# Kernel tuning notes

Hardware: AMD Instinct MI355X
Metric: run time of the kernel (lower is better)

The kernel has to match this reference:

```python
import jax, jax.numpy as jnp
import numpy as np

B, S, H, K, E, C = 4, 1024, 1024, 8, 512, 10000

def setup_inputs() -> dict:
    key = jax.random.key(0)
    ks = jax.random.split(key, 5)
    context = jax.random.normal(ks[0], (B, S, H), dtype=jnp.float32)
    prior_w = jax.random.normal(ks[1], (K, H), dtype=jnp.float32) * 0.02
    prior_b = jnp.zeros((K,), dtype=jnp.float32)
    latent_w = jax.random.normal(ks[2], (K * E, H), dtype=jnp.float32) * 0.02
    latent_b = jnp.zeros((K * E,), dtype=jnp.float32)
    dec_w = jax.random.normal(ks[3], (C, E), dtype=jnp.float32) * 0.02
    dec_b = jnp.zeros((C,), dtype=jnp.float32)
    return {"context": context, "prior_w": prior_w, "prior_b": prior_b,
            "latent_w": latent_w, "latent_b": latent_b,
            "dec_w": dec_w, "dec_b": dec_b}

def reference(context, prior_w, prior_b, latent_w, latent_b, dec_w, dec_b):
    # priors: softmax over components  [B,S,K]
    priors = jax.nn.softmax(jnp.einsum('bsh,kh->bsk', context, prior_w) + prior_b, axis=-1)
    # latent: [B,S,K,E] after tanh (dropout is identity at inference, dropoutl=0)
    latent = jnp.tanh((jnp.einsum('bsh,eh->bse', context, latent_w) + latent_b)
                      .reshape(B, S, K, E))
    # decoder logits + per-component softmax over classes  [B,S,K,C]
    probs = jax.nn.softmax(jnp.einsum('bske,ce->bskc', latent, dec_w) + dec_b, axis=-1)
    # mixture-weighted sum over components  [B,S,C]
    return jnp.einsum('bsk,bskc->bsc', priors, probs)
```

## Files before the change

### kernel.cpp

```cpp
#include <hip/hip_runtime.h>
#include <hip/hip_bf16.h>


#define BM 128
#define BN 128
#define BK 64

typedef __attribute__((ext_vector_type(8))) short bf16x8;
typedef __attribute__((ext_vector_type(4))) float f32x4;

typedef const __attribute__((address_space(1))) unsigned int* gas_u32p;
typedef __attribute__((address_space(3))) unsigned int* las_u32p;

__device__ __forceinline__ unsigned short f2bf(float x) {
  union { float f; unsigned int u; } un; un.f = x;
  unsigned int r = un.u + 0x7FFFu + ((un.u >> 16) & 1u);
  return (unsigned short)(r >> 16);
}

__global__ void k_cvt_bf16(const float4* __restrict__ src, ushort4* __restrict__ dst, int n4) {
  int i = blockIdx.x * blockDim.x + threadIdx.x;
  if (i < n4) {
    float4 v = src[i];
    ushort4 o;
    o.x = f2bf(v.x); o.y = f2bf(v.y); o.z = f2bf(v.z); o.w = f2bf(v.w);
    dst[i] = o;
  }
}

__global__ void k_priors(const float* __restrict__ ctx, const float* __restrict__ pw,
                         const float* __restrict__ pb, float* __restrict__ priors) {
  int t = blockIdx.x;
  int lane = threadIdx.x;
  __shared__ float logit[8];
  const float* c = ctx + (size_t)t * 1024;
  for (int k = 0; k < 8; ++k) {
    const float* w = pw + k * 1024;
    float s = 0.f;
    for (int h = lane; h < 1024; h += 64) s += c[h] * w[h];
    #pragma unroll
    for (int m = 1; m <= 32; m <<= 1) s += __shfl_xor(s, m);
    if (lane == 0) logit[k] = s + pb[k];
  }
  __syncthreads();
  if (lane == 0) {
    float mx = logit[0];
    for (int k = 1; k < 8; ++k) mx = fmaxf(mx, logit[k]);
    float z = 0.f, e[8];
    for (int k = 0; k < 8; ++k) { e[k] = __expf(logit[k] - mx); z += e[k]; }
    float inv = 1.f / z;
    for (int k = 0; k < 8; ++k) priors[(size_t)t * 8 + k] = e[k] * inv;
  }
}

__device__ __forceinline__ void gemm_mainloop(
    const unsigned short* __restrict__ A, const unsigned short* __restrict__ B,
    int lda, int ldb, int m0, int n0, int ktiles,
    unsigned short* ldsA, unsigned short* ldsB, f32x4 acc[4][4]) {
  const int tid = threadIdx.x;
  const int lane = tid & 63;
  const int wave = tid >> 6;
  const int wm = wave & 1, wn = wave >> 1;
  const int lrow = lane & 15, lq = lane >> 4;

  for (int kt = 0; kt < ktiles; ++kt) {
    int k0 = kt * BK;
    __syncthreads();
    #pragma unroll
    for (int p = 0; p < 4; ++p) {
      int chunk = p * 256 + tid;
      int row = chunk >> 3, kc = chunk & 7;
      int kcs = kc ^ (row & 7);
      __builtin_amdgcn_global_load_lds(
          (gas_u32p)(A + (size_t)(m0 + row) * lda + k0 + kcs * 8),
          (las_u32p)(ldsA + chunk * 8), 16, 0, 0);
      __builtin_amdgcn_global_load_lds(
          (gas_u32p)(B + (size_t)(n0 + row) * ldb + k0 + kcs * 8),
          (las_u32p)(ldsB + chunk * 8), 16, 0, 0);
    }
    __syncthreads();
    #pragma unroll
    for (int s = 0; s < 2; ++s) {
      int cbyteoff = (((s * 4 + lq) ^ (lrow & 7)) * 8);
      bf16x8 af[4], bfr[4];
      #pragma unroll
      for (int f = 0; f < 4; ++f)
        af[f] = *(const bf16x8*)(ldsA + (wm * 64 + f * 16 + lrow) * BK + cbyteoff);
      #pragma unroll
      for (int f = 0; f < 4; ++f)
        bfr[f] = *(const bf16x8*)(ldsB + (wn * 64 + f * 16 + lrow) * BK + cbyteoff);
      #pragma unroll
      for (int fi = 0; fi < 4; ++fi)
        #pragma unroll
        for (int fj = 0; fj < 4; ++fj)
          acc[fi][fj] = __builtin_amdgcn_mfma_f32_16x16x32_bf16(af[fi], bfr[fj], acc[fi][fj], 0, 0, 0);
    }
  }
}

__global__ __launch_bounds__(256, 4)
void k_latent(const unsigned short* __restrict__ ctxb, const unsigned short* __restrict__ lwb,
              const float* __restrict__ lb, unsigned short* __restrict__ latent) {
  __shared__ unsigned short lds[(BM + BN) * BK];
  f32x4 zero = {0.f, 0.f, 0.f, 0.f};
  f32x4 acc[4][4];
  #pragma unroll
  for (int i = 0; i < 4; ++i)
    #pragma unroll
    for (int j = 0; j < 4; ++j) acc[i][j] = zero;
  int l = blockIdx.x;
  int xcd = l & 7, idx = l >> 3;
  int ctl = idx & 3, by = idx >> 2;
  int m0 = by * BM, n0 = (xcd * 4 + ctl) * BN;
  gemm_mainloop(ctxb, lwb, 1024, 1024, m0, n0, 1024 / BK, lds, lds + BM * BK, acc);

  const int lane = threadIdx.x & 63, wave = threadIdx.x >> 6;
  const int wm = wave & 1, wn = wave >> 1, lrow = lane & 15, lq = lane >> 4;
  #pragma unroll
  for (int fi = 0; fi < 4; ++fi)
    #pragma unroll
    for (int fj = 0; fj < 4; ++fj) {
      int gcol = n0 + wn * 64 + fj * 16 + lrow;
      float bias = lb[gcol];
      #pragma unroll
      for (int r = 0; r < 4; ++r) {
        int grow = m0 + wm * 64 + fi * 16 + lq * 4 + r;
        float v = tanhf(acc[fi][fj][r] + bias);
        latent[(size_t)grow * 4096 + gcol] = f2bf(v);
      }
    }
}

__global__ __launch_bounds__(256, 4)
void k_dec_pass1(const unsigned short* __restrict__ latb, const unsigned short* __restrict__ dwb,
                 const float* __restrict__ db, float* __restrict__ Z) {
  __shared__ unsigned short lds[(BM + BN) * BK];
  int l = blockIdx.x;
  int xcd = l & 7, idx = l >> 3;
  int ctl = idx % 10, by = idx / 10;
  int n0 = (xcd * 10 + ctl) * BN, m0 = by * BM;
  if (n0 >= 10000) return;

  f32x4 zero = {0.f, 0.f, 0.f, 0.f};
  f32x4 acc[4][4];
  #pragma unroll
  for (int i = 0; i < 4; ++i)
    #pragma unroll
    for (int j = 0; j < 4; ++j) acc[i][j] = zero;
  gemm_mainloop(latb, dwb, 512, 512, m0, n0, 512 / BK, lds, lds + BM * BK, acc);

  const int lane = threadIdx.x & 63, wave = threadIdx.x >> 6;
  const int wm = wave & 1, wn = wave >> 1, lrow = lane & 15, lq = lane >> 4;
  float rowsum[4][4];
  #pragma unroll
  for (int fi = 0; fi < 4; ++fi)
    #pragma unroll
    for (int r = 0; r < 4; ++r) rowsum[fi][r] = 0.f;
  #pragma unroll
  for (int fj = 0; fj < 4; ++fj) {
    int gcol = n0 + wn * 64 + fj * 16 + lrow;
    bool valid = gcol < 10000;
    float bias = valid ? db[gcol] : 0.f;
    #pragma unroll
    for (int fi = 0; fi < 4; ++fi)
      #pragma unroll
      for (int r = 0; r < 4; ++r)
        if (valid) rowsum[fi][r] += __expf(acc[fi][fj][r] + bias);
  }
  #pragma unroll
  for (int fi = 0; fi < 4; ++fi)
    #pragma unroll
    for (int r = 0; r < 4; ++r) {
      float s = rowsum[fi][r];
      s += __shfl_xor(s, 1); s += __shfl_xor(s, 2);
      s += __shfl_xor(s, 4); s += __shfl_xor(s, 8);
      if (lrow == 0) atomicAdd(&Z[m0 + wm * 64 + fi * 16 + lq * 4 + r], s);
    }
}

__global__ __launch_bounds__(256, 4)
void k_dec_pass2(const unsigned short* __restrict__ latb, const unsigned short* __restrict__ dwb,
                 const float* __restrict__ db, const float* __restrict__ priors,
                 const float* __restrict__ Z, float* __restrict__ out) {
  __shared__ unsigned short lds[(BM + BN) * BK];
  int l = blockIdx.x;
  int xcd = l & 7, idx = l >> 3;
  int ctl = idx % 10, by = idx / 10;
  int n0 = (xcd * 10 + ctl) * BN, m0 = by * BM;
  if (n0 >= 10000) return;

  f32x4 zero = {0.f, 0.f, 0.f, 0.f};
  f32x4 acc[4][4];
  #pragma unroll
  for (int i = 0; i < 4; ++i)
    #pragma unroll
    for (int j = 0; j < 4; ++j) acc[i][j] = zero;
  gemm_mainloop(latb, dwb, 512, 512, m0, n0, 512 / BK, lds, lds + BM * BK, acc);

  const int tid = threadIdx.x;
  const int lane = tid & 63, wave = tid >> 6;
  const int wm = wave & 1, wn = wave >> 1, lrow = lane & 15, lq = lane >> 4;

  __syncthreads();
  float* ldsO = (float*)lds;

  #pragma unroll
  for (int fi = 0; fi < 4; ++fi) {
    int rbase = m0 + wm * 64 + fi * 16 + lq * 4;
    float w[4];
    #pragma unroll
    for (int r = 0; r < 4; ++r) w[r] = priors[rbase + r] / Z[rbase + r];
    #pragma unroll
    for (int fj = 0; fj < 4; ++fj) {
      int gcol = n0 + wn * 64 + fj * 16 + lrow;
      float bias = (gcol < 10000) ? db[gcol] : 0.f;
      float part = 0.f;
      #pragma unroll
      for (int r = 0; r < 4; ++r) part += w[r] * __expf(acc[fi][fj][r] + bias);
      float tok = part + __shfl_xor(part, 16);
      if (!(lq & 1)) {
        int tl = wm * 8 + fi * 2 + (lq >> 1);
        int cl = wn * 64 + fj * 16 + lrow;
        ldsO[tl * 128 + cl] = tok;
      }
    }
  }
  __syncthreads();
  int tok0 = m0 >> 3;
  #pragma unroll
  for (int it = 0; it < 2; ++it) {
    int f = it * 256 + tid;
    int tl = f >> 5, c4 = f & 31;
    int col = n0 + c4 * 4;
    if (col < 10000)
      *(float4*)(out + (size_t)(tok0 + tl) * 10000 + col) = *(float4*)(ldsO + tl * 128 + c4 * 4);
  }
}

extern "C" void kernel_launch(void* const* d_in, const int* in_sizes, int n_in,
                              void* d_out, int out_size, void* d_ws, size_t ws_size,
                              hipStream_t stream) {
  const float* ctx = (const float*)d_in[0];
  const float* pw  = (const float*)d_in[1];
  const float* pb  = (const float*)d_in[2];
  const float* lw  = (const float*)d_in[3];
  const float* lb  = (const float*)d_in[4];
  const float* dw  = (const float*)d_in[5];
  const float* db  = (const float*)d_in[6];
  float* out = (float*)d_out;

  char* ws = (char*)d_ws;
  unsigned short* ctxb = (unsigned short*)ws;
  unsigned short* lwb  = (unsigned short*)(ws + 8388608);
  unsigned short* dwb  = (unsigned short*)(ws + 16777216);
  unsigned short* latb = (unsigned short*)(ws + 27131904);
  float* priors        = (float*)(ws + 60686336);
  float* Z             = (float*)(ws + 60817408);

  k_cvt_bf16<<<4096, 256, 0, stream>>>((const float4*)ctx, (ushort4*)ctxb, 1048576);
  k_cvt_bf16<<<4096, 256, 0, stream>>>((const float4*)lw,  (ushort4*)lwb,  1048576);
  k_cvt_bf16<<<5000, 256, 0, stream>>>((const float4*)dw,  (ushort4*)dwb,  1280000);
  hipMemsetAsync(dwb + (size_t)10000 * 512, 0, (size_t)112 * 512 * 2, stream);
  hipMemsetAsync(Z, 0, 32768 * 4, stream);

  k_priors<<<4096, 64, 0, stream>>>(ctx, pw, pb, priors);
  k_latent<<<1024, 256, 0, stream>>>(ctxb, lwb, lb, latb);
  k_dec_pass1<<<20480, 256, 0, stream>>>(latb, dwb, db, Z);
  k_dec_pass2<<<20480, 256, 0, stream>>>(latb, dwb, db, priors, Z, out);
}
```

Measured before the change: 1.118 ms.

## Store fp16 exp logits in pass1 and combine instead of recomputing decoder GEMM

Pass 1 now writes the exponentiated decoder logits as fp16 into a large workspace buffer (about 660 MB), staged through LDS with a swizzle so the global stores coalesce. A new combine kernel reads these back and forms the prior-weighted normalized mixture, replacing the second decoder GEMM pass. This swaps recomputing a 32768x10000x512 GEMM for a large write plus read of the fp16 tensor. It only runs when the workspace is big enough, and fp16 storage of exp values risks overflow or precision loss.

```diff
diff --git a/kernel.cpp b/kernel.cpp
--- a/kernel.cpp
+++ b/kernel.cpp
@@ -8,6 +8,7 @@
 
 typedef __attribute__((ext_vector_type(8))) short bf16x8;
 typedef __attribute__((ext_vector_type(4))) float f32x4;
+typedef __attribute__((ext_vector_type(8))) _Float16 f16x8;
 
 typedef const __attribute__((address_space(1))) unsigned int* gas_u32p;
 typedef __attribute__((address_space(3))) unsigned int* las_u32p;
@@ -131,9 +132,11 @@
     }
 }
 
+template<int STORE>
 __global__ __launch_bounds__(256, 4)
 void k_dec_pass1(const unsigned short* __restrict__ latb, const unsigned short* __restrict__ dwb,
-                 const float* __restrict__ db, float* __restrict__ Z) {
+                 const float* __restrict__ db, float* __restrict__ Z,
+                 _Float16* __restrict__ P) {
   __shared__ unsigned short lds[(BM + BN) * BK];
   int l = blockIdx.x;
   int xcd = l & 7, idx = l >> 3;
@@ -151,6 +154,10 @@
 
   const int lane = threadIdx.x & 63, wave = threadIdx.x >> 6;
   const int wm = wave & 1, wn = wave >> 1, lrow = lane & 15, lq = lane >> 4;
+
+  if (STORE) __syncthreads();
+  _Float16* ldsP = (_Float16*)lds;
+
   float rowsum[4][4];
   #pragma unroll
   for (int fi = 0; fi < 4; ++fi)
@@ -164,9 +171,32 @@
     #pragma unroll
     for (int fi = 0; fi < 4; ++fi)
       #pragma unroll
-      for (int r = 0; r < 4; ++r)
-        if (valid) rowsum[fi][r] += __expf(acc[fi][fj][r] + bias);
-  }
+      for (int r = 0; r < 4; ++r) {
+        float e = __expf(acc[fi][fj][r] + bias);
+        if (STORE) {
+          _Float16 h = (_Float16)e;
+          if (valid) rowsum[fi][r] += (float)h;
+          int row_l = wm * 64 + fi * 16 + lq * 4 + r;
+          int col_l = wn * 64 + fj * 16 + lrow;
+          ldsP[row_l * 128 + (((col_l >> 3) ^ (row_l & 7)) << 3) + (col_l & 7)] = h;
+        } else {
+          if (valid) rowsum[fi][r] += e;
+        }
+      }
+  }
+
+  if (STORE) {
+    __syncthreads();
+    #pragma unroll
+    for (int it = 0; it < 8; ++it) {
+      int chunk = it * 256 + threadIdx.x;
+      int row_l = chunk >> 4, c8 = chunk & 15;
+      int slot = c8 ^ (row_l & 7);
+      uint4 v = *(const uint4*)((const char*)lds + row_l * 256 + slot * 16);
+      *(uint4*)(P + (size_t)(m0 + row_l) * 10112 + n0 + c8 * 8) = v;
+    }
+  }
+
   #pragma unroll
   for (int fi = 0; fi < 4; ++fi)
     #pragma unroll
@@ -176,6 +206,30 @@
       s += __shfl_xor(s, 4); s += __shfl_xor(s, 8);
       if (lrow == 0) atomicAdd(&Z[m0 + wm * 64 + fi * 16 + lq * 4 + r], s);
     }
+}
+
+__global__ __launch_bounds__(256)
+void k_combine(const _Float16* __restrict__ P, const float* __restrict__ priors,
+               const float* __restrict__ Z, float* __restrict__ out) {
+  int t = blockIdx.x;
+  const _Float16* base = P + (size_t)t * 8 * 10112;
+  float w[8];
+  #pragma unroll
+  for (int k = 0; k < 8; ++k) w[k] = priors[t * 8 + k] / Z[t * 8 + k];
+  for (int c8 = threadIdx.x; c8 < 1250; c8 += 256) {
+    int c = c8 * 8;
+    float s[8] = {0.f, 0.f, 0.f, 0.f, 0.f, 0.f, 0.f, 0.f};
+    #pragma unroll
+    for (int k = 0; k < 8; ++k) {
+      f16x8 v = *(const f16x8*)(base + (size_t)k * 10112 + c);
+      #pragma unroll
+      for (int j = 0; j < 8; ++j) s[j] += w[k] * (float)v[j];
+    }
+    float4 o0 = {s[0], s[1], s[2], s[3]};
+    float4 o1 = {s[4], s[5], s[6], s[7]};
+    *(float4*)(out + (size_t)t * 10000 + c) = o0;
+    *(float4*)(out + (size_t)t * 10000 + c + 4) = o1;
+  }
 }
 
 __global__ __launch_bounds__(256, 4)
@@ -256,6 +310,9 @@
   unsigned short* latb = (unsigned short*)(ws + 27131904);
   float* priors        = (float*)(ws + 60686336);
   float* Z             = (float*)(ws + 60817408);
+  _Float16* Pex        = (_Float16*)(ws + 60948480);
+  const size_t WS_NEED_STORE = 60948480ull + 662700032ull;
+  const bool store_path = ws_size >= WS_NEED_STORE;
 
   k_cvt_bf16<<<4096, 256, 0, stream>>>((const float4*)ctx, (ushort4*)ctxb, 1048576);
   k_cvt_bf16<<<4096, 256, 0, stream>>>((const float4*)lw,  (ushort4*)lwb,  1048576);
@@ -265,6 +322,11 @@
 
   k_priors<<<4096, 64, 0, stream>>>(ctx, pw, pb, priors);
   k_latent<<<1024, 256, 0, stream>>>(ctxb, lwb, lb, latb);
-  k_dec_pass1<<<20480, 256, 0, stream>>>(latb, dwb, db, Z);
-  k_dec_pass2<<<20480, 256, 0, stream>>>(latb, dwb, db, priors, Z, out);
-}
+  if (store_path) {
+    k_dec_pass1<1><<<20480, 256, 0, stream>>>(latb, dwb, db, Z, Pex);
+    k_combine<<<4096, 256, 0, stream>>>(Pex, priors, Z, out);
+  } else {
+    k_dec_pass1<0><<<20480, 256, 0, stream>>>(latb, dwb, db, Z, nullptr);
+    k_dec_pass2<<<20480, 256, 0, stream>>>(latb, dwb, db, priors, Z, out);
+  }
+}
```

Result: no change. 1.115 ms (-0.2%).
